# Kernel tuning notes

Measured on AMD Instinct MI355X. Metric: run time of the kernel, lower is better.

The kernel has to match this reference:

```python
import jax, jax.numpy as jnp
import numpy as np

B, H, W, C = 32, 64, 64, 256
WS, SHIFT = 8, 4
HIDDEN = 4 * C
EPS = 1e-5


def layer_norm(x, g, b):
    mu = jnp.mean(x, axis=-1, keepdims=True)
    var = jnp.mean(jnp.square(x - mu), axis=-1, keepdims=True)
    return (x - mu) * jax.lax.rsqrt(var + EPS) * g + b


def window_partition(x, ws):
    # x: [B, H, W, C] -> [B*nH*nW, ws*ws, C]
    b, h, w, c = x.shape
    x = x.reshape(b, h // ws, ws, w // ws, ws, c)
    return x.transpose(0, 1, 3, 2, 4, 5).reshape(-1, ws * ws, c)


def window_reverse(xw, ws, h, w):
    # xw: [B*nH*nW, ws, ws, C] -> [B, H, W, C]
    b = xw.shape[0] // ((h // ws) * (w // ws))
    x = xw.reshape(b, h // ws, w // ws, ws, ws, -1)
    return x.transpose(0, 1, 3, 2, 4, 5).reshape(b, h, w, -1)


def setup_inputs() -> dict:
    key = jax.random.key(0)
    ks = jax.random.split(key, 5)
    s = 0.02
    return {
        "x": jax.random.normal(ks[0], (B, H * W, C), dtype=jnp.float32),
        "ln1_g": jnp.ones((C,), jnp.float32),
        "ln1_b": jnp.zeros((C,), jnp.float32),
        "ln2_g": jnp.ones((C,), jnp.float32),
        "ln2_b": jnp.zeros((C,), jnp.float32),
        "w1": jax.random.normal(ks[1], (C, HIDDEN), jnp.float32) * s,
        "b1": jnp.zeros((HIDDEN,), jnp.float32),
        "w2": jax.random.normal(ks[2], (HIDDEN, C), jnp.float32) * s,
        "b2": jnp.zeros((C,), jnp.float32),
    }


def reference(x, ln1_g, ln1_b, ln2_g, ln2_b, w1, b1, w2, b2):
    shortcut = x
    h = layer_norm(x, ln1_g, ln1_b)          # [B, L, C]
    h = h.reshape(B, H, W, C)
    # cyclic shift (SW-MSA path, shift_size > 0)
    h = jnp.roll(h, shift=(-SHIFT, -SHIFT), axis=(1, 2))
    xw = window_partition(h, WS)             # [nW*B, WS*WS, C]
    attn_w = xw                              # self.attn = nn.Identity() in source
    attn_w = attn_w.reshape(-1, WS, WS, C)
    h = window_reverse(attn_w, WS, H, W)     # [B, H, W, C]
    h = jnp.roll(h, shift=(SHIFT, SHIFT), axis=(1, 2))
    h = h.reshape(B, H * W, C)
    x = shortcut + h                         # drop_path = 0 -> identity
    # MLP: fc1 -> GELU(exact) -> fc2 (dropout = 0)
    m = layer_norm(x, ln2_g, ln2_b)
    m = jax.nn.gelu(jnp.einsum('blc,ch->blh', m, w1) + b1, approximate=False)
    m = jnp.einsum('blh,hc->blc', m, w2) + b2
    return x + m
```

## Files before the change

kernel.cpp:

```cpp
#include <hip/hip_runtime.h>
#include <hip/hip_bf16.h>

#define M_TOTAL (32 * 64 * 64)
#define CDIM 256
#define HDIM 1024

typedef float  floatx4 __attribute__((ext_vector_type(4)));
typedef short  short8  __attribute__((ext_vector_type(8)));

__global__ __launch_bounds__(256) void frag_pack(
    const float* __restrict__ src, __hip_bfloat16* __restrict__ dst,
    int K, int N)
{
    const int idx  = blockIdx.x * 256 + threadIdx.x;
    const int lane = idx & 63;
    const int nkk  = K >> 5;
    const int kk   = (idx >> 6) % nkk;
    const int g    = idx / (nkk << 6);
    const int col  = g * 16 + (lane & 15);
    const int k0   = kk * 32 + (lane >> 4) * 8;
    union { short8 v; __hip_bfloat16 h[8]; } p;
#pragma unroll
    for (int e = 0; e < 8; ++e)
        p.h[e] = __float2bfloat16(src[(long)(k0 + e) * N + col]);
    ((short8*)dst)[idx] = p.v;
}

__device__ __forceinline__ float gelu_fast(float v)
{
    const float t = v * __builtin_fmaf(v * v, 0.044715f, 1.0f);
    const float e = __expf(t * -1.5957691216f);
    return v * __builtin_amdgcn_rcpf(1.0f + e);
}

__global__ __launch_bounds__(512, 4) void swin_fused(
    const float* __restrict__ x,
    const float* __restrict__ ln1g, const float* __restrict__ ln1b,
    const float* __restrict__ ln2g, const float* __restrict__ ln2b,
    const short8* __restrict__ w1f, const float* __restrict__ fb1,
    const short8* __restrict__ w2f, const float* __restrict__ fb2,
    float* __restrict__ xnbuf, float* __restrict__ out)
{
    __shared__ __align__(16) __hip_bfloat16 As[16384];
    __shared__ __align__(16) __hip_bfloat16 Hs[2][8192];

    const int  tid = threadIdx.x;
    const long m0  = (long)blockIdx.x * 64;

    {
        const int row  = tid >> 3;
        const int part = tid & 7;
        const float* xr = x + (m0 + row) * CDIM + part * 32;

        float4 v[8];
        float s = 0.f, sq = 0.f;
#pragma unroll
        for (int i = 0; i < 8; ++i) {
            v[i] = ((const float4*)xr)[i];
            s  += v[i].x + v[i].y + v[i].z + v[i].w;
            sq += v[i].x*v[i].x + v[i].y*v[i].y + v[i].z*v[i].z + v[i].w*v[i].w;
        }
        s  += __shfl_xor(s, 1);  s  += __shfl_xor(s, 2);  s  += __shfl_xor(s, 4);
        sq += __shfl_xor(sq, 1); sq += __shfl_xor(sq, 2); sq += __shfl_xor(sq, 4);
        const float mu = s * (1.f / CDIM);
        const float rs = rsqrtf(sq * (1.f / CDIM) - mu * mu + 1e-5f);

        float s2 = 0.f, q2 = 0.f;
        float* xnp = xnbuf + (m0 + row) * CDIM + part * 32;
#pragma unroll
        for (int i = 0; i < 8; ++i) {
            const float4 G = ((const float4*)(ln1g + part * 32))[i];
            const float4 B = ((const float4*)(ln1b + part * 32))[i];
            v[i].x += (v[i].x - mu) * rs * G.x + B.x;
            v[i].y += (v[i].y - mu) * rs * G.y + B.y;
            v[i].z += (v[i].z - mu) * rs * G.z + B.z;
            v[i].w += (v[i].w - mu) * rs * G.w + B.w;
            s2 += v[i].x + v[i].y + v[i].z + v[i].w;
            q2 += v[i].x*v[i].x + v[i].y*v[i].y + v[i].z*v[i].z + v[i].w*v[i].w;
            ((float4*)xnp)[i] = v[i];
        }
        s2 += __shfl_xor(s2, 1); s2 += __shfl_xor(s2, 2); s2 += __shfl_xor(s2, 4);
        q2 += __shfl_xor(q2, 1); q2 += __shfl_xor(q2, 2); q2 += __shfl_xor(q2, 4);
        const float mu2 = s2 * (1.f / CDIM);
        const float rs2 = rsqrtf(q2 * (1.f / CDIM) - mu2 * mu2 + 1e-5f);

#pragma unroll
        for (int i = 0; i < 8; ++i) {
            const int col0 = part * 32 + i * 4;
            const float4 G = ((const float4*)(ln2g + part * 32))[i];
            const float4 B = ((const float4*)(ln2b + part * 32))[i];
            union { ushort4 u; __hip_bfloat16 h[4]; } p;
            p.h[0] = __float2bfloat16((v[i].x - mu2) * rs2 * G.x + B.x);
            p.h[1] = __float2bfloat16((v[i].y - mu2) * rs2 * G.y + B.y);
            p.h[2] = __float2bfloat16((v[i].z - mu2) * rs2 * G.z + B.z);
            p.h[3] = __float2bfloat16((v[i].w - mu2) * rs2 * G.w + B.w);
            const int idx16 = ((col0 >> 5) * 4 + ((col0 >> 3) & 3)) * 64 + row;
            *(ushort4*)(As + idx16 * 8 + (col0 & 7)) = p.u;
        }
    }
    __syncthreads();

    const int wn = tid >> 6;
    const int lane = tid & 63;
    const int fr = lane & 15, fq = lane >> 4;

    floatx4 acc2[4][2] = {};

    float fb2w[2];
#pragma unroll
    for (int nf = 0; nf < 2; ++nf) fb2w[nf] = fb2[wn * 32 + nf * 16 + fr];


#pragma unroll 2
    for (int c = 0; c < 8; ++c) {
        const short8* p1 = w1f + ((c * 8 + wn) * 8) * 64 + lane;
        const float bb1 = fb1[c * 128 + wn * 16 + fr];

        floatx4 acc1[4];
#pragma unroll
        for (int mf = 0; mf < 4; ++mf) acc1[mf] = (floatx4){0.f, 0.f, 0.f, 0.f};
#pragma unroll
        for (int kf = 0; kf < 8; ++kf) {
            const short8 b = p1[kf * 64];
            short8 a[4];
#pragma unroll
            for (int mf = 0; mf < 4; ++mf)
                a[mf] = *(const short8*)(As + ((kf * 4 + fq) * 64 + mf * 16 + fr) * 8);
#pragma unroll
            for (int mf = 0; mf < 4; ++mf)
                acc1[mf] = __builtin_amdgcn_mfma_f32_16x16x32_bf16(
                    a[mf], b, acc1[mf], 0, 0, 0);
        }

        {
            __hip_bfloat16* hb = Hs[c & 1];
            const int col = wn * 16 + fr;
            __hip_bfloat16* hp =
                hb + (((col >> 5) * 4 + ((col >> 3) & 3)) * 64) * 8 + (col & 7);
#pragma unroll
            for (int mf = 0; mf < 4; ++mf)
#pragma unroll
                for (int j = 0; j < 4; ++j) {
                    const int row = mf * 16 + fq * 4 + j;
                    hp[row * 8] = __float2bfloat16(gelu_fast(acc1[mf][j] + bb1));
                }
        }
        __syncthreads();

        const __hip_bfloat16* hb = Hs[c & 1];
#pragma unroll
        for (int kf = 0; kf < 4; ++kf) {
            short8 bw[2];
#pragma unroll
            for (int nf = 0; nf < 2; ++nf)
                bw[nf] = w2f[((wn * 2 + nf) * 32 + c * 4 + kf) * 64 + lane];
            short8 ha[4];
#pragma unroll
            for (int mf = 0; mf < 4; ++mf)
                ha[mf] = *(const short8*)(hb + ((kf * 4 + fq) * 64 + mf * 16 + fr) * 8);
#pragma unroll
            for (int mf = 0; mf < 4; ++mf)
#pragma unroll
                for (int nf = 0; nf < 2; ++nf)
                    acc2[mf][nf] = __builtin_amdgcn_mfma_f32_16x16x32_bf16(
                        ha[mf], bw[nf], acc2[mf][nf], 0, 0, 0);
        }
    }

#pragma unroll
    for (int nf = 0; nf < 2; ++nf) {
        const int oc = wn * 32 + nf * 16 + fr;
#pragma unroll
        for (int mf = 0; mf < 4; ++mf)
#pragma unroll
            for (int j = 0; j < 4; ++j) {
                const long row = m0 + mf * 16 + fq * 4 + j;
                out[row * CDIM + oc] = acc2[mf][nf][j] + fb2w[nf]
                                     + xnbuf[row * CDIM + oc];
            }
    }
}

extern "C" void kernel_launch(void* const* d_in, const int* in_sizes, int n_in,
                              void* d_out, int out_size, void* d_ws, size_t ws_size,
                              hipStream_t stream)
{
    const float* x    = (const float*)d_in[0];
    const float* ln1g = (const float*)d_in[1];
    const float* ln1b = (const float*)d_in[2];
    const float* ln2g = (const float*)d_in[3];
    const float* ln2b = (const float*)d_in[4];
    const float* w1   = (const float*)d_in[5];
    const float* b1   = (const float*)d_in[6];
    const float* w2   = (const float*)d_in[7];
    const float* b2   = (const float*)d_in[8];
    float* out = (float*)d_out;

    char* ws = (char*)d_ws;
    float*          xnbuf = (float*)ws;
    __hip_bfloat16* w1fb  = (__hip_bfloat16*)(ws + 134217728);
    __hip_bfloat16* w2fb  = (__hip_bfloat16*)(ws + 134742016);

    frag_pack<<<128, 256, 0, stream>>>(w1, w1fb, CDIM, HDIM);
    frag_pack<<<128, 256, 0, stream>>>(w2, w2fb, HDIM, CDIM);

    swin_fused<<<M_TOTAL / 64, 512, 0, stream>>>(
        x, ln1g, ln1b, ln2g, ln2b,
        (const short8*)w1fb, b1, (const short8*)w2fb, b2, xnbuf, out);
}
```

Measured before the change: 322.7 us.

## Warp-specialize fused MLP into producer and consumer waves with software pipelining

Splits the 8 waves into 4 producer waves that compute fc1+GELU chunks into the double-buffered LDS tile and 4 consumer waves that run fc2 on the previous chunk, skewed by one iteration. The aim is to overlap the two GEMM phases and cut the barrier stalls between them, with one sync per step. In exchange each wave holds larger accumulator tiles (acc2 grows to 4x4), which raises register pressure and may hurt occupancy under launch_bounds(512,4). The work per wave is also unbalanced, since fc1 and fc2 per chunk may differ in cost.

```diff
diff --git a/kernel.cpp b/kernel.cpp
--- a/kernel.cpp
+++ b/kernel.cpp
@@ -100,84 +100,105 @@
     }
     __syncthreads();
 
-    const int wn = tid >> 6;
+    const int wave = tid >> 6;
     const int lane = tid & 63;
     const int fr = lane & 15, fq = lane >> 4;
-
-    floatx4 acc2[4][2] = {};
-
-    float fb2w[2];
-#pragma unroll
-    for (int nf = 0; nf < 2; ++nf) fb2w[nf] = fb2[wn * 32 + nf * 16 + fr];
-
-
-#pragma unroll 2
-    for (int c = 0; c < 8; ++c) {
-        const short8* p1 = w1f + ((c * 8 + wn) * 8) * 64 + lane;
-        const float bb1 = fb1[c * 128 + wn * 16 + fr];
-
-        floatx4 acc1[4];
-#pragma unroll
-        for (int mf = 0; mf < 4; ++mf) acc1[mf] = (floatx4){0.f, 0.f, 0.f, 0.f};
-#pragma unroll
-        for (int kf = 0; kf < 8; ++kf) {
-            const short8 b = p1[kf * 64];
-            short8 a[4];
+    const bool producer = (wave < 4);
+    const int  pw = wave;
+    const int  cw = wave - 4;
+
+    floatx4 acc2[4][4] = {};
+
+    float fb2w[4];
+#pragma unroll
+    for (int nf = 0; nf < 4; ++nf)
+        fb2w[nf] = fb2[((cw < 0 ? 0 : cw) * 64 + nf * 16 + fr) & 255];
+
+#pragma unroll 1
+    for (int c = 0; c <= 8; ++c) {
+        if (producer) {
+            if (c < 8) {
+                floatx4 acc1[4][2];
+#pragma unroll
+                for (int mf = 0; mf < 4; ++mf)
+#pragma unroll
+                    for (int nf = 0; nf < 2; ++nf)
+                        acc1[mf][nf] = (floatx4){0.f, 0.f, 0.f, 0.f};
+#pragma unroll
+                for (int kf = 0; kf < 8; ++kf) {
+                    short8 b[2];
+#pragma unroll
+                    for (int nf = 0; nf < 2; ++nf)
+                        b[nf] = w1f[((c * 8 + pw * 2 + nf) * 8 + kf) * 64 + lane];
+                    short8 a[4];
+#pragma unroll
+                    for (int mf = 0; mf < 4; ++mf)
+                        a[mf] = *(const short8*)(
+                            As + ((kf * 4 + fq) * 64 + mf * 16 + fr) * 8);
+#pragma unroll
+                    for (int mf = 0; mf < 4; ++mf)
+#pragma unroll
+                        for (int nf = 0; nf < 2; ++nf)
+                            acc1[mf][nf] = __builtin_amdgcn_mfma_f32_16x16x32_bf16(
+                                a[mf], b[nf], acc1[mf][nf], 0, 0, 0);
+                }
+                __hip_bfloat16* hb = Hs[c & 1];
+#pragma unroll
+                for (int nf = 0; nf < 2; ++nf) {
+                    const int col = pw * 32 + nf * 16 + fr;
+                    const float bb1 = fb1[c * 128 + col];
+                    __hip_bfloat16* hp =
+                        hb + (((col >> 5) * 4 + ((col >> 3) & 3)) * 64) * 8 + (col & 7);
+#pragma unroll
+                    for (int mf = 0; mf < 4; ++mf)
+#pragma unroll
+                        for (int j = 0; j < 4; ++j) {
+                            const int row = mf * 16 + fq * 4 + j;
+                            hp[row * 8] =
+                                __float2bfloat16(gelu_fast(acc1[mf][nf][j] + bb1));
+                        }
+                }
+            }
+        } else {
+            if (c >= 1) {
+                const int cc = c - 1;
+                const __hip_bfloat16* hb = Hs[cc & 1];
+#pragma unroll
+                for (int kf = 0; kf < 4; ++kf) {
+                    short8 bw[4];
+#pragma unroll
+                    for (int nf = 0; nf < 4; ++nf)
+                        bw[nf] = w2f[((cw * 4 + nf) * 32 + cc * 4 + kf) * 64 + lane];
+                    short8 ha[4];
+#pragma unroll
+                    for (int mf = 0; mf < 4; ++mf)
+                        ha[mf] = *(const short8*)(
+                            hb + ((kf * 4 + fq) * 64 + mf * 16 + fr) * 8);
+#pragma unroll
+                    for (int mf = 0; mf < 4; ++mf)
+#pragma unroll
+                        for (int nf = 0; nf < 4; ++nf)
+                            acc2[mf][nf] = __builtin_amdgcn_mfma_f32_16x16x32_bf16(
+                                ha[mf], bw[nf], acc2[mf][nf], 0, 0, 0);
+                }
+            }
+        }
+        __syncthreads();
+    }
+
+    if (!producer) {
+#pragma unroll
+        for (int nf = 0; nf < 4; ++nf) {
+            const int oc = cw * 64 + nf * 16 + fr;
 #pragma unroll
             for (int mf = 0; mf < 4; ++mf)
-                a[mf] = *(const short8*)(As + ((kf * 4 + fq) * 64 + mf * 16 + fr) * 8);
-#pragma unroll
-            for (int mf = 0; mf < 4; ++mf)
-                acc1[mf] = __builtin_amdgcn_mfma_f32_16x16x32_bf16(
-                    a[mf], b, acc1[mf], 0, 0, 0);
-        }
-
-        {
-            __hip_bfloat16* hb = Hs[c & 1];
-            const int col = wn * 16 + fr;
-            __hip_bfloat16* hp =
-                hb + (((col >> 5) * 4 + ((col >> 3) & 3)) * 64) * 8 + (col & 7);
-#pragma unroll
-            for (int mf = 0; mf < 4; ++mf)
 #pragma unroll
                 for (int j = 0; j < 4; ++j) {
-                    const int row = mf * 16 + fq * 4 + j;
-                    hp[row * 8] = __float2bfloat16(gelu_fast(acc1[mf][j] + bb1));
-                }
-        }
-        __syncthreads();
-
-        const __hip_bfloat16* hb = Hs[c & 1];
-#pragma unroll
-        for (int kf = 0; kf < 4; ++kf) {
-            short8 bw[2];
-#pragma unroll
-            for (int nf = 0; nf < 2; ++nf)
-                bw[nf] = w2f[((wn * 2 + nf) * 32 + c * 4 + kf) * 64 + lane];
-            short8 ha[4];
-#pragma unroll
-            for (int mf = 0; mf < 4; ++mf)
-                ha[mf] = *(const short8*)(hb + ((kf * 4 + fq) * 64 + mf * 16 + fr) * 8);
-#pragma unroll
-            for (int mf = 0; mf < 4; ++mf)
-#pragma unroll
-                for (int nf = 0; nf < 2; ++nf)
-                    acc2[mf][nf] = __builtin_amdgcn_mfma_f32_16x16x32_bf16(
-                        ha[mf], bw[nf], acc2[mf][nf], 0, 0, 0);
-        }
-    }
-
-#pragma unroll
-    for (int nf = 0; nf < 2; ++nf) {
-        const int oc = wn * 32 + nf * 16 + fr;
-#pragma unroll
-        for (int mf = 0; mf < 4; ++mf)
-#pragma unroll
-            for (int j = 0; j < 4; ++j) {
-                const long row = m0 + mf * 16 + fq * 4 + j;
-                out[row * CDIM + oc] = acc2[mf][nf][j] + fb2w[nf]
-                                     + xnbuf[row * CDIM + oc];
-            }
+                    const long row = m0 + mf * 16 + fq * 4 + j;
+                    out[row * CDIM + oc] = acc2[mf][nf][j] + fb2w[nf]
+                                         + xnbuf[row * CDIM + oc];
+                }
+        }
     }
 }
 
```

Result: slower. 484.2 us (+50.0%).
